# Kernel tuning notes

Hardware: AMD Instinct MI355X
Metric: run time of the kernel (lower is better)

Reference implementation:

```python
import jax, jax.numpy as jnp
import numpy as np

N = 8192      # num nodes (pad index == N, matching the original's 15004 sentinel)
IN = 128; H = 128; OUT = 128
T = 512       # number of teams
L = 30        # max_len
SAMPLE = 5    # sample team size
DCAT = 2 * H + OUT


def _glorot(k, shape):
    lim = np.sqrt(6.0 / (shape[0] + shape[1]))
    return jax.random.uniform(k, shape, jnp.float32, -lim, lim)


def setup_inputs() -> dict:
    key = jax.random.key(0)
    ks = jax.random.split(key, 32)
    x = jax.random.normal(ks[0], (1, N, IN), jnp.float32)
    # sparse-ish binary dense adjacency, avg degree ~16 (memory-bound adj@x)
    adj = (jax.random.uniform(ks[1], (1, N, N), jnp.float32) < 16.0 / N).astype(jnp.float32)
    # team index matrix, ragged lengths in [SAMPLE+1, L], padded with N
    lens = jax.random.randint(ks[2], (T,), SAMPLE + 1, L + 1)
    ids = jax.random.randint(ks[3], (T, L), 0, N)
    teams = jnp.where(jnp.arange(L)[None, :] < lens[:, None], ids, N)
    # DenseGraphConv params: lin_rel (W,b) on adj@x, lin_root (no bias) on x
    p = dict(
        W1r=_glorot(ks[4], (IN, H)), b1=jnp.zeros((H,), jnp.float32), W1s=_glorot(ks[5], (IN, H)),
        W2r=_glorot(ks[6], (H, H)), b2=jnp.zeros((H,), jnp.float32), W2s=_glorot(ks[7], (H, H)),
        W3r=_glorot(ks[8], (H, OUT)), b3=jnp.zeros((OUT,), jnp.float32), W3s=_glorot(ks[9], (H, OUT)),
        g1=jnp.ones((H,), jnp.float32), be1=jnp.zeros((H,), jnp.float32),
        g2=jnp.ones((H,), jnp.float32), be2=jnp.zeros((H,), jnp.float32),
        g3=jnp.ones((OUT,), jnp.float32), be3=jnp.zeros((OUT,), jnp.float32),
        Wl=_glorot(ks[10], (DCAT, OUT)), bl=jnp.zeros((OUT,), jnp.float32),
        att=_glorot(ks[11], (T, L)),  # xavier_uniform'd attention vectors
    )
    return dict(x=x, adj=adj, teams=teams, sample_len=SAMPLE, **p)


def _bn(h, g, b):
    # BatchNorm1d in training mode over flattened (B*N, C), biased variance
    B, n, C = h.shape
    h2 = h.reshape(-1, C)
    mu = h2.mean(0)
    var = h2.var(0)
    return (((h2 - mu) * jax.lax.rsqrt(var + 1e-5)) * g + b).reshape(B, n, C)


def _conv(x, adj, Wr, br, Ws):
    # DenseGraphConv: lin_rel(adj @ x) + lin_root(x)
    return jnp.einsum('bnm,bmf,fo->bno', adj, x, Wr) + br + jnp.einsum('bnf,fo->bno', x, Ws)


def reference(x, adj, teams, sample_len, W1r, b1, W1s, W2r, b2, W2s, W3r, b3, W3s,
              g1, be1, g2, be2, g3, be3, Wl, bl, att):
    x1 = _bn(jax.nn.relu(_conv(x, adj, W1r, b1, W1s)), g1, be1)
    x2 = _bn(jax.nn.relu(_conv(x1, adj, W2r, b2, W2s)), g2, be2)
    x3 = _bn(jax.nn.relu(_conv(x2, adj, W3r, b3, W3s)), g3, be3)
    xcat = jnp.concatenate([x1, x2, x3], axis=-1)               # [1,N,DCAT]
    s = jax.nn.relu(xcat @ Wl + bl)
    appended = jnp.concatenate([xcat[0], jnp.zeros((1, xcat.shape[-1]), xcat.dtype)], 0)  # [N+1,D]
    gathered = appended[teams]                                   # [T,L,D] ragged gather
    # team: full softmax over attention vector (pad positions keep softmax mass,
    # but gather the zero row -> contribute zero, matching the original)
    a_team = jax.nn.softmax(att, axis=-1)
    team_emb = jnp.einsum('tl,tld->td', a_team, gathered)
    pos = jnp.arange(teams.shape[1])[None, :]
    # sample: sub-softmax over the attention entries at the sample members' positions
    m_s = pos < sample_len
    a_s = jax.nn.softmax(jnp.where(m_s, att, -1e30), axis=-1)
    sample_emb = jnp.einsum('tl,tld->td', a_s, gathered)
    # remain: team minus sample minus pad sentinel
    m_r = (pos >= sample_len) & (teams != N)
    a_r = jax.nn.softmax(jnp.where(m_r, att, -1e30), axis=-1)
    remain_emb = jnp.einsum('tl,tld->td', a_r, gathered)
    return s, xcat, team_emb, sample_emb, remain_emb
```

## Files before the change

### kernel.cpp

```cpp
#include <hip/hip_runtime.h>
#include <stdint.h>

#define NN 8192
#define CC 128
#define TT 512
#define LL 30
#define CAP 64

typedef unsigned int uint32;
typedef unsigned long long ull;
typedef unsigned short u16;

typedef float f32x4 __attribute__((ext_vector_type(4)));
typedef short bf16x8 __attribute__((ext_vector_type(8)));

#define STAT_SCALE 1048576.0f
#define STAT_INV (1.0f / 1048576.0f)

__device__ __forceinline__ float bf2f(uint32 h) { return __uint_as_float(h << 16); }
__device__ __forceinline__ u16 f2bf(float f) {
    uint32 u = __float_as_uint(f);
    u = (u + 0x7fffu + ((u >> 16) & 1u)) >> 16;
    return (u16)u;
}
__device__ __forceinline__ uint32 pack2(float a, float b) {
    return (uint32)f2bf(a) | ((uint32)f2bf(b) << 16);
}
__device__ __forceinline__ void coef_from_stats(const ull* __restrict__ st, int c,
                                                const float* __restrict__ g,
                                                const float* __restrict__ be,
                                                float& ca, float& cb) {
    float s = (float)(long long)st[c] * STAT_INV;
    float q = (float)(long long)st[128 + c] * STAT_INV;
    float mu = s * (1.f / NN);
    float var = q * (1.f / NN) - mu * mu;
    float rs = rsqrtf(var + 1e-5f);
    ca = g[c] * rs;
    cb = be[c] - mu * ca;
}

__global__ __launch_bounds__(256) void k_pre(
    const float* __restrict__ adj,
    const float* __restrict__ W1r, const float* __restrict__ W1s,
    const float* __restrict__ W2r, const float* __restrict__ W2s,
    const float* __restrict__ W3r, const float* __restrict__ W3s,
    const float* __restrict__ Wl, const float* __restrict__ x0,
    int* __restrict__ nbr, int* __restrict__ cnt,
    u16* __restrict__ wfrag,
    u16* __restrict__ yp1, u16* __restrict__ yp2, u16* __restrict__ yp3,
    u16* __restrict__ Abraw, ull* __restrict__ statsAcc) {
    int b = blockIdx.x, tid = threadIdx.x;
    if (b < 2048) {
        int row = b * 4 + (tid >> 6);
        int lane = tid & 63;
        const float4* arow = (const float4*)(adj + (size_t)row * NN);
        int base = 0;
        int* dst = nbr + (size_t)row * CAP;
        for (int it = 0; it < 32; it += 4) {
            float4 v0 = arow[it * 64 + lane];
            float4 v1 = arow[it * 64 + 64 + lane];
            float4 v2 = arow[it * 64 + 128 + lane];
            float4 v3 = arow[it * 64 + 192 + lane];
            float4 vs[4] = {v0, v1, v2, v3};
#pragma unroll
            for (int u = 0; u < 4; ++u) {
                uint32 m4 = (vs[u].x != 0.f ? 1u : 0u) | (vs[u].y != 0.f ? 2u : 0u) |
                            (vs[u].z != 0.f ? 4u : 0u) | (vs[u].w != 0.f ? 8u : 0u);
                int c4 = __popc(m4);
                int p = c4;
#pragma unroll
                for (int off = 1; off < 64; off <<= 1) {
                    int t = __shfl_up(p, off);
                    if (lane >= off) p += t;
                }
                int pos = base + p - c4;
                int colb = (it + u) * 256 + lane * 4;
                if (m4 & 1u) { if (pos < CAP) dst[pos] = colb;     pos++; }
                if (m4 & 2u) { if (pos < CAP) dst[pos] = colb + 1; pos++; }
                if (m4 & 4u) { if (pos < CAP) dst[pos] = colb + 2; pos++; }
                if (m4 & 8u) { if (pos < CAP) dst[pos] = colb + 3; }
                base += __shfl(p, 63);
            }
        }
        int nn = base < CAP ? base : CAP;
        int npad = (nn + 3) & ~3;
        for (int p = nn + lane; p < npad; p += 64) dst[p] = NN;
        if (lane == 0) cnt[row] = nn;
        int c = lane * 2;
        float a0 = 0.f, a1 = 0.f;
        for (int j = 0; j < npad; j += 4) {
            int4 m = *(const int4*)(dst + j);
            if (m.x < NN) { float2 v = *(const float2*)(x0 + (size_t)m.x * CC + c); a0 += v.x; a1 += v.y; }
            if (m.y < NN) { float2 v = *(const float2*)(x0 + (size_t)m.y * CC + c); a0 += v.x; a1 += v.y; }
            if (m.z < NN) { float2 v = *(const float2*)(x0 + (size_t)m.z * CC + c); a0 += v.x; a1 += v.y; }
            if (m.w < NN) { float2 v = *(const float2*)(x0 + (size_t)m.w * CC + c); a0 += v.x; a1 += v.y; }
        }
        *(uint32*)(Abraw + (size_t)row * CC + c) = pack2(a0, a1);
    } else if (b < 2336) {
        int bb = b - 2048;
        const float* Wa;
        const float* Wb;
        int tile, gbase;
        if (bb < 64)       { Wa = W1r; Wb = W1s; tile = bb;       gbase = 0; }
        else if (bb < 128) { Wa = W2r; Wb = W2s; tile = bb - 64;  gbase = 64; }
        else if (bb < 192) { Wa = W3r; Wb = W3s; tile = bb - 128; gbase = 128; }
        else               { Wa = Wl;  Wb = nullptr; tile = bb - 192; gbase = 192; }
        int kt = tile >> 3, nt = tile & 7;
        int lane = tid & 63, i0 = (tid >> 6) * 2;
        int n = nt * 16 + (lane & 15);
        u16* dst = wfrag + ((size_t)(gbase + tile) * 64 + lane) * 8;
#pragma unroll
        for (int ii = 0; ii < 2; ++ii) {
            int i = i0 + ii;
            int k = kt * 32 + ((lane >> 4) * 8) + i;
            float v;
            if (Wb) v = (k < 128) ? Wa[k * CC + n] : Wb[(k - 128) * CC + n];
            else    v = Wa[k * CC + n];
            dst[i] = f2bf(v);
        }
    } else {
        if (tid < 128) {
            yp1[(size_t)NN * CC + tid] = 0;
            yp2[(size_t)NN * CC + tid] = 0;
            yp3[(size_t)NN * CC + tid] = 0;
#pragma unroll
            for (int l = 0; l < 3; ++l) {
                statsAcc[l * 256 + tid] = 0ull;
                statsAcc[l * 256 + 128 + tid] = 0ull;
            }
        }
    }
}

__global__ __launch_bounds__(256) void k_agg(const u16* __restrict__ src,
                                             const int* __restrict__ nbr,
                                             const int* __restrict__ cnt,
                                             u16* __restrict__ Abraw) {
    int row = blockIdx.x * 4 + (threadIdx.x >> 6);
    int lane = threadIdx.x & 63;
    int c = lane * 2;
    int nreal = cnt[row];
    int npad = (nreal + 3) & ~3;
    const int* nb = nbr + (size_t)row * CAP;
    float a0 = 0.f, a1 = 0.f;
    for (int j = 0; j < npad; j += 4) {
        int4 m = *(const int4*)(nb + j);
        uint32 v0 = *(const uint32*)(src + (size_t)m.x * CC + c);
        uint32 v1 = *(const uint32*)(src + (size_t)m.y * CC + c);
        uint32 v2 = *(const uint32*)(src + (size_t)m.z * CC + c);
        uint32 v3 = *(const uint32*)(src + (size_t)m.w * CC + c);
        a0 += bf2f(v0 & 0xffffu); a1 += bf2f(v0 >> 16);
        a0 += bf2f(v1 & 0xffffu); a1 += bf2f(v1 >> 16);
        a0 += bf2f(v2 & 0xffffu); a1 += bf2f(v2 >> 16);
        a0 += bf2f(v3 & 0xffffu); a1 += bf2f(v3 >> 16);
    }
    *(uint32*)(Abraw + (size_t)row * CC + c) = pack2(a0, a1);
}

template <int LAYER>
__global__ __launch_bounds__(512) void k_gemm(const u16* __restrict__ Abraw,
                                              const float* __restrict__ x0,
                                              const u16* __restrict__ yprev,
                                              const int* __restrict__ cnt,
                                              const u16* __restrict__ wfrag,
                                              const float* __restrict__ bias,
                                              const ull* __restrict__ statsPrev,
                                              const float* __restrict__ g,
                                              const float* __restrict__ be,
                                              ull* __restrict__ statsOut,
                                              u16* __restrict__ yp) {
    __shared__ u16 A[32][264];
    __shared__ float sSum[CC], sSq[CC];
    __shared__ alignas(16) float cA[CC];
    __shared__ alignas(16) float cB[CC];
    int tid = threadIdx.x, lane = tid & 63, wid = tid >> 6;
    int row0 = blockIdx.x * 32;
    if (tid < CC) {
        sSum[tid] = 0.f; sSq[tid] = 0.f;
        if constexpr (LAYER > 1) {
            float a, b;
            coef_from_stats(statsPrev, tid, g, be, a, b);
            cA[tid] = a; cB[tid] = b;
        }
    }
    __syncthreads();
    for (int i = tid; i < 1024; i += 512) {
        int r = i >> 5, k = (i & 31) * 8;
        int row = row0 + r;
        uint4 o;
        if constexpr (LAYER == 1) {
            if (k < 128) {
                o = *(const uint4*)(Abraw + (size_t)row * CC + k);
            } else {
                int c = k - 128;
                float4 v0 = *(const float4*)(x0 + (size_t)row * CC + c);
                float4 v1 = *(const float4*)(x0 + (size_t)row * CC + c + 4);
                o.x = pack2(v0.x, v0.y); o.y = pack2(v0.z, v0.w);
                o.z = pack2(v1.x, v1.y); o.w = pack2(v1.z, v1.w);
            }
        } else {
            uint4 raw;
            float fn;
            int c;
            if (k < 128) {
                c = k;
                raw = *(const uint4*)(Abraw + (size_t)row * CC + k);
                fn = (float)cnt[row];
            } else {
                c = k - 128;
                raw = *(const uint4*)(yprev + (size_t)row * CC + c);
                fn = 1.f;
            }
            float4 a0 = *(const float4*)(cA + c);
            float4 a1 = *(const float4*)(cA + c + 4);
            float4 b0 = *(const float4*)(cB + c);
            float4 b1 = *(const float4*)(cB + c + 4);
            o.x = pack2(a0.x * bf2f(raw.x & 0xffffu) + b0.x * fn, a0.y * bf2f(raw.x >> 16) + b0.y * fn);
            o.y = pack2(a0.z * bf2f(raw.y & 0xffffu) + b0.z * fn, a0.w * bf2f(raw.y >> 16) + b0.w * fn);
            o.z = pack2(a1.x * bf2f(raw.z & 0xffffu) + b1.x * fn, a1.y * bf2f(raw.z >> 16) + b1.y * fn);
            o.w = pack2(a1.z * bf2f(raw.w & 0xffffu) + b1.z * fn, a1.w * bf2f(raw.w >> 16) + b1.w * fn);
        }
        *(uint4*)&A[r][k] = o;
    }
    __syncthreads();

    int mh = wid >> 2, nh = wid & 3;
    int arow = mh * 16 + (lane & 15);
    int kg = (lane >> 4) * 8;
    f32x4 acc[2];
#pragma unroll
    for (int nt = 0; nt < 2; ++nt) acc[nt] = (f32x4){0.f, 0.f, 0.f, 0.f};
#pragma unroll
    for (int kt = 0; kt < 8; ++kt) {
        bf16x8 a = *(const bf16x8*)&A[arow][kt * 32 + kg];
        const u16* wb = wfrag + ((size_t)(kt * 8 + nh * 2) * 64 + lane) * 8;
#pragma unroll
        for (int nt = 0; nt < 2; ++nt) {
            bf16x8 bfr = *(const bf16x8*)(wb + (size_t)nt * 512);
            acc[nt] = __builtin_amdgcn_mfma_f32_16x16x32_bf16(a, bfr, acc[nt], 0, 0, 0);
        }
    }
    int rowb = row0 + mh * 16 + ((lane >> 4) * 4);
#pragma unroll
    for (int nt = 0; nt < 2; ++nt) {
        int col = nh * 32 + nt * 16 + (lane & 15);
        float bv = bias[col];
        float s1 = 0.f, s2 = 0.f;
#pragma unroll
        for (int q = 0; q < 4; ++q) {
            float y = acc[nt][q] + bv;
            y = y > 0.f ? y : 0.f;
            yp[(size_t)(rowb + q) * CC + col] = f2bf(y);
            s1 += y;
            s2 += y * y;
        }
        s1 += __shfl_xor(s1, 16); s1 += __shfl_xor(s1, 32);
        s2 += __shfl_xor(s2, 16); s2 += __shfl_xor(s2, 32);
        if ((lane >> 4) == 0) { atomicAdd(&sSum[col], s1); atomicAdd(&sSq[col], s2); }
    }
    __syncthreads();
    if (tid < 128) {
        atomicAdd(statsOut + tid, (ull)(long long)llrintf(sSum[tid] * STAT_SCALE));
    } else if (tid < 256) {
        atomicAdd(statsOut + tid, (ull)(long long)llrintf(sSq[tid - 128] * STAT_SCALE));
    }
}

__global__ __launch_bounds__(256) void k_out(
    const u16* __restrict__ yp1, const u16* __restrict__ yp2, const u16* __restrict__ yp3,
    const ull* __restrict__ statsAcc,
    const float* __restrict__ g1, const float* __restrict__ be1,
    const float* __restrict__ g2, const float* __restrict__ be2,
    const float* __restrict__ g3, const float* __restrict__ be3,
    const u16* __restrict__ wfL, const float* __restrict__ bias,
    const int* __restrict__ teams, const int* __restrict__ slen_p,
    const float* __restrict__ att,
    float* __restrict__ sout, float* __restrict__ xcat,
    float* __restrict__ oT, float* __restrict__ oS, float* __restrict__ oR) {
    __shared__ alignas(16) char pool[12544];
    __shared__ alignas(16) float cAll[768];
    int b = blockIdx.x, tid = threadIdx.x;
    if (tid < 128) {
        const float* gs[3] = {g1, g2, g3};
        const float* bes[3] = {be1, be2, be3};
#pragma unroll
        for (int l = 0; l < 3; ++l) {
            float a, bb;
            coef_from_stats(statsAcc + l * 256, tid, gs[l], bes[l], a, bb);
            cAll[l * 256 + tid] = a;
            cAll[l * 256 + 128 + tid] = bb;
        }
    }
    __syncthreads();
    const u16* yps[3] = {yp1, yp2, yp3};
    if (b < 512) {
        u16 (*A)[392] = (u16(*)[392])pool;
        int lane = tid & 63, wid = tid >> 6;
        int row0 = b * 16;
        for (int i = tid; i < 768; i += 256) {
            int r = i / 48, kk = (i % 48) * 8;
            int seg = kk >> 7, c = kk & 127;
            uint4 raw = *(const uint4*)(yps[seg] + (size_t)(row0 + r) * CC + c);
            const float* cf = cAll + seg * 256;
            float4 av0 = *(const float4*)(cf + c);
            float4 av1 = *(const float4*)(cf + c + 4);
            float4 bv0 = *(const float4*)(cf + 128 + c);
            float4 bv1 = *(const float4*)(cf + 128 + c + 4);
            uint4 o;
            o.x = pack2(av0.x * bf2f(raw.x & 0xffffu) + bv0.x, av0.y * bf2f(raw.x >> 16) + bv0.y);
            o.y = pack2(av0.z * bf2f(raw.y & 0xffffu) + bv0.z, av0.w * bf2f(raw.y >> 16) + bv0.w);
            o.z = pack2(av1.x * bf2f(raw.z & 0xffffu) + bv1.x, av1.y * bf2f(raw.z >> 16) + bv1.y);
            o.w = pack2(av1.z * bf2f(raw.w & 0xffffu) + bv1.z, av1.w * bf2f(raw.w >> 16) + bv1.w);
            *(uint4*)&A[r][kk] = o;
        }
        __syncthreads();
        int nh = wid;
        int arow = lane & 15;
        int kg = (lane >> 4) * 8;
        f32x4 acc[2];
#pragma unroll
        for (int nt = 0; nt < 2; ++nt) acc[nt] = (f32x4){0.f, 0.f, 0.f, 0.f};
#pragma unroll
        for (int kt = 0; kt < 12; ++kt) {
            bf16x8 a = *(const bf16x8*)&A[arow][kt * 32 + kg];
            const u16* wb = wfL + ((size_t)(kt * 8 + nh * 2) * 64 + lane) * 8;
#pragma unroll
            for (int nt = 0; nt < 2; ++nt) {
                bf16x8 bfr = *(const bf16x8*)(wb + (size_t)nt * 512);
                acc[nt] = __builtin_amdgcn_mfma_f32_16x16x32_bf16(a, bfr, acc[nt], 0, 0, 0);
            }
        }
        int rowb = row0 + ((lane >> 4) * 4);
#pragma unroll
        for (int nt = 0; nt < 2; ++nt) {
            int col = nh * 32 + nt * 16 + (lane & 15);
            float bv = bias[col];
#pragma unroll
            for (int q = 0; q < 4; ++q) {
                float y = acc[nt][q] + bv;
                sout[(size_t)(rowb + q) * CC + col] = y > 0.f ? y : 0.f;
            }
        }
    } else if (b < 1024) {
        float* wT = (float*)pool;
        float* wS = wT + 32;
        float* wR = wS + 32;
        int* ids = (int*)(wR + 32);
        int t = b - 512;
        if (tid < 64) {
            int lane = tid;
            bool act = lane < LL;
            float a = act ? att[t * LL + lane] : 0.f;
            int id = act ? teams[t * LL + lane] : NN;
            if (act) ids[lane] = id;
            int sl = *slen_p;
            const float NEG = -1e30f;
            float v = act ? a : NEG;
#pragma unroll
            for (int o = 32; o > 0; o >>= 1) v = fmaxf(v, __shfl_xor(v, o));
            float mT = v;
            float eT = act ? __expf(a - mT) : 0.f;
            v = eT;
#pragma unroll
            for (int o = 32; o > 0; o >>= 1) v += __shfl_xor(v, o);
            float sT = v;
            bool inS = act && (lane < sl);
            v = inS ? a : NEG;
#pragma unroll
            for (int o = 32; o > 0; o >>= 1) v = fmaxf(v, __shfl_xor(v, o));
            float mS = v;
            float eS = inS ? __expf(a - mS) : 0.f;
            v = eS;
#pragma unroll
            for (int o = 32; o > 0; o >>= 1) v += __shfl_xor(v, o);
            float sS = v;
            bool inR = act && (lane >= sl) && (id != NN);
            v = inR ? a : NEG;
#pragma unroll
            for (int o = 32; o > 0; o >>= 1) v = fmaxf(v, __shfl_xor(v, o));
            float mR = v;
            float eR = inR ? __expf(a - mR) : 0.f;
            v = eR;
#pragma unroll
            for (int o = 32; o > 0; o >>= 1) v += __shfl_xor(v, o);
            float sR = v;
            if (act) {
                wT[lane] = eT / sT;
                wS[lane] = eS / sS;
                wR[lane] = eR / sR;
            }
        }
        __syncthreads();
        for (int d = tid; d < 384; d += 256) {
            int seg = d >> 7, c = d & 127;
            const u16* xb = yps[seg];
            float ca = cAll[seg * 256 + c];
            float cb = cAll[seg * 256 + 128 + c];
            float aT = 0.f, aS = 0.f, aR = 0.f;
            for (int l = 0; l < LL; ++l) {
                int id = ids[l];
                if (id < NN) {
                    float vv = ca * bf2f((uint32)xb[(size_t)id * CC + c]) + cb;
                    aT += wT[l] * vv;
                    aS += wS[l] * vv;
                    aR += wR[l] * vv;
                }
            }
            oT[(size_t)t * 384 + d] = aT;
            oS[(size_t)t * 384 + d] = aS;
            oR[(size_t)t * 384 + d] = aR;
        }
    } else {
        int idx = (b - 1024) * 256 + tid;
        int n = idx / 96;
        int k = (idx % 96) * 4;
        int seg = k >> 7, c = k & 127;
        ushort4 raw = *(const ushort4*)(yps[seg] + (size_t)n * CC + c);
        const float* cf = cAll + seg * 256;
        float4 a = *(const float4*)(cf + c);
        float4 bb = *(const float4*)(cf + 128 + c);
        float4 o;
        o.x = a.x * bf2f((uint32)raw.x) + bb.x;
        o.y = a.y * bf2f((uint32)raw.y) + bb.y;
        o.z = a.z * bf2f((uint32)raw.z) + bb.z;
        o.w = a.w * bf2f((uint32)raw.w) + bb.w;
        *(float4*)(xcat + (size_t)n * 384 + k) = o;
    }
}

extern "C" void kernel_launch(void* const* d_in, const int* in_sizes, int n_in,
                              void* d_out, int out_size, void* d_ws, size_t ws_size,
                              hipStream_t stream) {
    const float* x = (const float*)d_in[0];
    const float* adj = (const float*)d_in[1];
    const int* teams = (const int*)d_in[2];
    const int* slen = (const int*)d_in[3];
    const float* W1r = (const float*)d_in[4];
    const float* b1 = (const float*)d_in[5];
    const float* W1s = (const float*)d_in[6];
    const float* W2r = (const float*)d_in[7];
    const float* b2 = (const float*)d_in[8];
    const float* W2s = (const float*)d_in[9];
    const float* W3r = (const float*)d_in[10];
    const float* b3 = (const float*)d_in[11];
    const float* W3s = (const float*)d_in[12];
    const float* g1 = (const float*)d_in[13];
    const float* be1 = (const float*)d_in[14];
    const float* g2 = (const float*)d_in[15];
    const float* be2 = (const float*)d_in[16];
    const float* g3 = (const float*)d_in[17];
    const float* be3 = (const float*)d_in[18];
    const float* Wl = (const float*)d_in[19];
    const float* bl = (const float*)d_in[20];
    const float* att = (const float*)d_in[21];

    float* out = (float*)d_out;
    float* s_out = out;
    float* xcat = out + (size_t)NN * CC;
    float* oT = xcat + (size_t)NN * 384;
    float* oS = oT + (size_t)TT * 384;
    float* oR = oS + (size_t)TT * 384;

    char* ws = (char*)d_ws;
    size_t off = 0;
    int* nbr = (int*)(ws + off); off += (size_t)NN * CAP * 4;
    int* cnt = (int*)(ws + off); off += (size_t)NN * 4;
    u16* yp1 = (u16*)(ws + off); off += (size_t)(NN + 1) * CC * 2;
    u16* yp2 = (u16*)(ws + off); off += (size_t)(NN + 1) * CC * 2;
    u16* yp3 = (u16*)(ws + off); off += (size_t)(NN + 1) * CC * 2;
    u16* Abraw = (u16*)(ws + off); off += (size_t)NN * CC * 2;
    u16* wfrag = (u16*)(ws + off); off += (size_t)288 * 512 * 2;
    ull* statsAcc = (ull*)(ws + off); off += (size_t)768 * 8;

    k_pre<<<2337, 256, 0, stream>>>(adj, W1r, W1s, W2r, W2s, W3r, W3s, Wl, x,
                                    nbr, cnt, wfrag, yp1, yp2, yp3, Abraw, statsAcc);
    k_gemm<1><<<256, 512, 0, stream>>>(Abraw, x, nullptr, cnt, wfrag, b1,
                                       nullptr, nullptr, nullptr, statsAcc, yp1);
    k_agg<<<2048, 256, 0, stream>>>(yp1, nbr, cnt, Abraw);
    k_gemm<2><<<256, 512, 0, stream>>>(Abraw, nullptr, yp1, cnt, wfrag + 64 * 512, b2,
                                       statsAcc, g1, be1, statsAcc + 256, yp2);
    k_agg<<<2048, 256, 0, stream>>>(yp2, nbr, cnt, Abraw);
    k_gemm<3><<<256, 512, 0, stream>>>(Abraw, nullptr, yp2, cnt, wfrag + 128 * 512, b3,
                                       statsAcc + 256, g2, be2, statsAcc + 512, yp3);
    k_out<<<4096, 256, 0, stream>>>(yp1, yp2, yp3, statsAcc,
                                    g1, be1, g2, be2, g3, be3,
                                    wfrag + 192 * 512, bl, teams, slen, att,
                                    s_out, xcat, oT, oS, oR);
}
```

Measured before the change: 130.1 us.

## Fuse neighbor aggregation into layer 2/3 GEMM prologue, drop k_agg launches

Removes the separate k_agg kernels for layers 2 and 3. Each wave of the GEMM block now gathers and sums neighbor rows for four of its rows directly into shared memory, applying the BN affine transform inline. This cuts two kernel launches and the round trip of the aggregated matrix through global memory. In exchange the GEMM grid of 256 blocks now carries the latency-bound gather with less parallelism than the former 2048-block aggregation kernel, and branches per row inside each wave may diverge.

```diff
diff --git a/kernel.cpp b/kernel.cpp
--- a/kernel.cpp
+++ b/kernel.cpp
@@ -132,35 +132,11 @@
     }
 }
 
-__global__ __launch_bounds__(256) void k_agg(const u16* __restrict__ src,
-                                             const int* __restrict__ nbr,
-                                             const int* __restrict__ cnt,
-                                             u16* __restrict__ Abraw) {
-    int row = blockIdx.x * 4 + (threadIdx.x >> 6);
-    int lane = threadIdx.x & 63;
-    int c = lane * 2;
-    int nreal = cnt[row];
-    int npad = (nreal + 3) & ~3;
-    const int* nb = nbr + (size_t)row * CAP;
-    float a0 = 0.f, a1 = 0.f;
-    for (int j = 0; j < npad; j += 4) {
-        int4 m = *(const int4*)(nb + j);
-        uint32 v0 = *(const uint32*)(src + (size_t)m.x * CC + c);
-        uint32 v1 = *(const uint32*)(src + (size_t)m.y * CC + c);
-        uint32 v2 = *(const uint32*)(src + (size_t)m.z * CC + c);
-        uint32 v3 = *(const uint32*)(src + (size_t)m.w * CC + c);
-        a0 += bf2f(v0 & 0xffffu); a1 += bf2f(v0 >> 16);
-        a0 += bf2f(v1 & 0xffffu); a1 += bf2f(v1 >> 16);
-        a0 += bf2f(v2 & 0xffffu); a1 += bf2f(v2 >> 16);
-        a0 += bf2f(v3 & 0xffffu); a1 += bf2f(v3 >> 16);
-    }
-    *(uint32*)(Abraw + (size_t)row * CC + c) = pack2(a0, a1);
-}
-
 template <int LAYER>
 __global__ __launch_bounds__(512) void k_gemm(const u16* __restrict__ Abraw,
                                               const float* __restrict__ x0,
                                               const u16* __restrict__ yprev,
+                                              const int* __restrict__ nbr,
                                               const int* __restrict__ cnt,
                                               const u16* __restrict__ wfrag,
                                               const float* __restrict__ bias,
@@ -184,11 +160,12 @@
         }
     }
     __syncthreads();
-    for (int i = tid; i < 1024; i += 512) {
-        int r = i >> 5, k = (i & 31) * 8;
-        int row = row0 + r;
-        uint4 o;
-        if constexpr (LAYER == 1) {
+
+    if constexpr (LAYER == 1) {
+        for (int i = tid; i < 1024; i += 512) {
+            int r = i >> 5, k = (i & 31) * 8;
+            int row = row0 + r;
+            uint4 o;
             if (k < 128) {
                 o = *(const uint4*)(Abraw + (size_t)row * CC + k);
             } else {
@@ -198,29 +175,87 @@
                 o.x = pack2(v0.x, v0.y); o.y = pack2(v0.z, v0.w);
                 o.z = pack2(v1.x, v1.y); o.w = pack2(v1.z, v1.w);
             }
-        } else {
-            uint4 raw;
-            float fn;
-            int c;
-            if (k < 128) {
-                c = k;
-                raw = *(const uint4*)(Abraw + (size_t)row * CC + k);
-                fn = (float)cnt[row];
-            } else {
-                c = k - 128;
-                raw = *(const uint4*)(yprev + (size_t)row * CC + c);
-                fn = 1.f;
-            }
-            float4 a0 = *(const float4*)(cA + c);
-            float4 a1 = *(const float4*)(cA + c + 4);
-            float4 b0 = *(const float4*)(cB + c);
-            float4 b1 = *(const float4*)(cB + c + 4);
-            o.x = pack2(a0.x * bf2f(raw.x & 0xffffu) + b0.x * fn, a0.y * bf2f(raw.x >> 16) + b0.y * fn);
-            o.y = pack2(a0.z * bf2f(raw.y & 0xffffu) + b0.z * fn, a0.w * bf2f(raw.y >> 16) + b0.w * fn);
-            o.z = pack2(a1.x * bf2f(raw.z & 0xffffu) + b1.x * fn, a1.y * bf2f(raw.z >> 16) + b1.y * fn);
-            o.w = pack2(a1.z * bf2f(raw.w & 0xffffu) + b1.z * fn, a1.w * bf2f(raw.w >> 16) + b1.w * fn);
-        }
-        *(uint4*)&A[r][k] = o;
+            *(uint4*)&A[r][k] = o;
+        }
+    } else {
+        int r0 = wid * 4;
+        int g0 = row0 + r0;
+        int n0 = cnt[g0], n1 = cnt[g0 + 1], n2 = cnt[g0 + 2], n3 = cnt[g0 + 3];
+        int p0 = (n0 + 3) & ~3, p1 = (n1 + 3) & ~3, p2 = (n2 + 3) & ~3, p3 = (n3 + 3) & ~3;
+        const int* nb0 = nbr + (size_t)g0 * CAP;
+        const int* nb1 = nb0 + CAP;
+        const int* nb2 = nb1 + CAP;
+        const int* nb3 = nb2 + CAP;
+        int c = lane * 2;
+        float a00 = 0.f, a01 = 0.f, a10 = 0.f, a11 = 0.f;
+        float a20 = 0.f, a21 = 0.f, a30 = 0.f, a31 = 0.f;
+        int jm = max(max(p0, p1), max(p2, p3));
+        for (int j = 0; j < jm; j += 4) {
+            if (j < p0) {
+                int4 m = *(const int4*)(nb0 + j);
+                uint32 v0 = *(const uint32*)(yprev + (size_t)m.x * CC + c);
+                uint32 v1 = *(const uint32*)(yprev + (size_t)m.y * CC + c);
+                uint32 v2 = *(const uint32*)(yprev + (size_t)m.z * CC + c);
+                uint32 v3 = *(const uint32*)(yprev + (size_t)m.w * CC + c);
+                a00 += bf2f(v0 & 0xffffu); a01 += bf2f(v0 >> 16);
+                a00 += bf2f(v1 & 0xffffu); a01 += bf2f(v1 >> 16);
+                a00 += bf2f(v2 & 0xffffu); a01 += bf2f(v2 >> 16);
+                a00 += bf2f(v3 & 0xffffu); a01 += bf2f(v3 >> 16);
+            }
+            if (j < p1) {
+                int4 m = *(const int4*)(nb1 + j);
+                uint32 v0 = *(const uint32*)(yprev + (size_t)m.x * CC + c);
+                uint32 v1 = *(const uint32*)(yprev + (size_t)m.y * CC + c);
+                uint32 v2 = *(const uint32*)(yprev + (size_t)m.z * CC + c);
+                uint32 v3 = *(const uint32*)(yprev + (size_t)m.w * CC + c);
+                a10 += bf2f(v0 & 0xffffu); a11 += bf2f(v0 >> 16);
+                a10 += bf2f(v1 & 0xffffu); a11 += bf2f(v1 >> 16);
+                a10 += bf2f(v2 & 0xffffu); a11 += bf2f(v2 >> 16);
+                a10 += bf2f(v3 & 0xffffu); a11 += bf2f(v3 >> 16);
+            }
+            if (j < p2) {
+                int4 m = *(const int4*)(nb2 + j);
+                uint32 v0 = *(const uint32*)(yprev + (size_t)m.x * CC + c);
+                uint32 v1 = *(const uint32*)(yprev + (size_t)m.y * CC + c);
+                uint32 v2 = *(const uint32*)(yprev + (size_t)m.z * CC + c);
+                uint32 v3 = *(const uint32*)(yprev + (size_t)m.w * CC + c);
+                a20 += bf2f(v0 & 0xffffu); a21 += bf2f(v0 >> 16);
+                a20 += bf2f(v1 & 0xffffu); a21 += bf2f(v1 >> 16);
+                a20 += bf2f(v2 & 0xffffu); a21 += bf2f(v2 >> 16);
+                a20 += bf2f(v3 & 0xffffu); a21 += bf2f(v3 >> 16);
+            }
+            if (j < p3) {
+                int4 m = *(const int4*)(nb3 + j);
+                uint32 v0 = *(const uint32*)(yprev + (size_t)m.x * CC + c);
+                uint32 v1 = *(const uint32*)(yprev + (size_t)m.y * CC + c);
+                uint32 v2 = *(const uint32*)(yprev + (size_t)m.z * CC + c);
+                uint32 v3 = *(const uint32*)(yprev + (size_t)m.w * CC + c);
+                a30 += bf2f(v0 & 0xffffu); a31 += bf2f(v0 >> 16);
+                a30 += bf2f(v1 & 0xffffu); a31 += bf2f(v1 >> 16);
+                a30 += bf2f(v2 & 0xffffu); a31 += bf2f(v2 >> 16);
+                a30 += bf2f(v3 & 0xffffu); a31 += bf2f(v3 >> 16);
+            }
+        }
+        float ca0 = cA[c], ca1 = cA[c + 1], cb0 = cB[c], cb1 = cB[c + 1];
+        *(uint32*)&A[r0 + 0][c] = pack2(ca0 * a00 + cb0 * (float)n0, ca1 * a01 + cb1 * (float)n0);
+        *(uint32*)&A[r0 + 1][c] = pack2(ca0 * a10 + cb0 * (float)n1, ca1 * a11 + cb1 * (float)n1);
+        *(uint32*)&A[r0 + 2][c] = pack2(ca0 * a20 + cb0 * (float)n2, ca1 * a21 + cb1 * (float)n2);
+        *(uint32*)&A[r0 + 3][c] = pack2(ca0 * a30 + cb0 * (float)n3, ca1 * a31 + cb1 * (float)n3);
+        {
+            int r = tid >> 4;
+            int ch = (tid & 15) * 8;
+            uint4 raw = *(const uint4*)(yprev + (size_t)(row0 + r) * CC + ch);
+            float4 A0 = *(const float4*)(cA + ch);
+            float4 A1 = *(const float4*)(cA + ch + 4);
+            float4 B0 = *(const float4*)(cB + ch);
+            float4 B1 = *(const float4*)(cB + ch + 4);
+            uint4 o;
+            o.x = pack2(A0.x * bf2f(raw.x & 0xffffu) + B0.x, A0.y * bf2f(raw.x >> 16) + B0.y);
+            o.y = pack2(A0.z * bf2f(raw.y & 0xffffu) + B0.z, A0.w * bf2f(raw.y >> 16) + B0.w);
+            o.z = pack2(A1.x * bf2f(raw.z & 0xffffu) + B1.x, A1.y * bf2f(raw.z >> 16) + B1.y);
+            o.w = pack2(A1.z * bf2f(raw.w & 0xffffu) + B1.z, A1.w * bf2f(raw.w >> 16) + B1.w);
+            *(uint4*)&A[r][128 + ch] = o;
+        }
     }
     __syncthreads();
 
@@ -474,13 +509,11 @@
 
     k_pre<<<2337, 256, 0, stream>>>(adj, W1r, W1s, W2r, W2s, W3r, W3s, Wl, x,
                                     nbr, cnt, wfrag, yp1, yp2, yp3, Abraw, statsAcc);
-    k_gemm<1><<<256, 512, 0, stream>>>(Abraw, x, nullptr, cnt, wfrag, b1,
+    k_gemm<1><<<256, 512, 0, stream>>>(Abraw, x, nullptr, nbr, cnt, wfrag, b1,
                                        nullptr, nullptr, nullptr, statsAcc, yp1);
-    k_agg<<<2048, 256, 0, stream>>>(yp1, nbr, cnt, Abraw);
-    k_gemm<2><<<256, 512, 0, stream>>>(Abraw, nullptr, yp1, cnt, wfrag + 64 * 512, b2,
+    k_gemm<2><<<256, 512, 0, stream>>>(nullptr, nullptr, yp1, nbr, cnt, wfrag + 64 * 512, b2,
                                        statsAcc, g1, be1, statsAcc + 256, yp2);
-    k_agg<<<2048, 256, 0, stream>>>(yp2, nbr, cnt, Abraw);
-    k_gemm<3><<<256, 512, 0, stream>>>(Abraw, nullptr, yp2, cnt, wfrag + 128 * 512, b3,
+    k_gemm<3><<<256, 512, 0, stream>>>(nullptr, nullptr, yp2, nbr, cnt, wfrag + 128 * 512, b3,
                                        statsAcc + 256, g2, be2, statsAcc + 512, yp3);
     k_out<<<4096, 256, 0, stream>>>(yp1, yp2, yp3, statsAcc,
                                     g1, be1, g2, be2, g3, be3,
```

New measurement: 134.3 us. 1.03x slower.
